# Optimization experiments

Measured on AMD Instinct MI355X. Metric: run time of the kernel, lower is better.

Reference implementation:

```python
import jax, jax.numpy as jnp
import numpy as np

B, K, D = 8, 1024, 512
H, DQ, DV = 8, 64, 64


def setup_inputs() -> dict:
    key = jax.random.key(0)
    ks = jax.random.split(key, 11)
    s = 0.02  # param init scale
    return {
        "query": jax.random.normal(ks[0], (B, K, D), jnp.float32),
        "key": jax.random.normal(ks[1], (B, K, D), jnp.float32),
        "value": jax.random.normal(ks[2], (B, K, D), jnp.float32),
        "Wq": jax.random.normal(ks[3], (D, H * DQ), jnp.float32) * s,
        "bq": jax.random.normal(ks[4], (H * DQ,), jnp.float32) * s,
        "Wk": jax.random.normal(ks[5], (D, H * DQ), jnp.float32) * s,
        "bk": jax.random.normal(ks[6], (H * DQ,), jnp.float32) * s,
        "Wv": jax.random.normal(ks[7], (D, H * DV), jnp.float32) * s,
        "bv": jax.random.normal(ks[8], (H * DV,), jnp.float32) * s,
        "Wo": jax.random.normal(ks[9], (H * DV, D), jnp.float32) * s,
        "bo": jax.random.normal(ks[10], (D,), jnp.float32) * s,
    }


def reference(query, key, value, Wq, bq, Wk, bk, Wv, bv, Wo, bo):
    b, k, _ = query.shape
    # Linear projections, split into heads: chunk(h, dim=-1) + cat(dim=0)
    # is equivalent to reshape (b, k, h, d) with head on a separate axis.
    q = (query @ Wq + bq).reshape(b, k, H, DQ)  # b k h dq
    kk = (key @ Wk + bk).reshape(b, k, H, DQ)   # b k h dq
    v = (value @ Wv + bv).reshape(b, k, H, DV)  # b k h dv
    # NOTE: original scales by sqrt(K) (sequence length), not sqrt(dq).
    scale = 1.0 / jnp.sqrt(jnp.asarray(k, q.dtype))
    scores = jnp.einsum("bqhd,bkhd->bhqk", q, kk) * scale
    attn = jax.nn.softmax(scores, axis=-1)
    ctx = jnp.einsum("bhqk,bkhd->bqhd", attn, v).reshape(b, k, H * DV)
    return ctx @ Wo + bo
```

## Files before the change

kernel.cpp:

```cpp
#include <hip/hip_runtime.h>
#include <hip/hip_bf16.h>

#define DEVI __device__ __forceinline__

typedef __attribute__((ext_vector_type(4))) float f32x4;
typedef __attribute__((ext_vector_type(8))) short bf16x8;

static constexpr int BB  = 8;
static constexpr int SEQ = 1024;
static constexpr int DIM = 512;
static constexpr int NH  = 8;
static constexpr int HD  = 64;
static constexpr int M   = BB * SEQ;


DEVI unsigned short f2bf(float x) {
  unsigned int u = __builtin_bit_cast(unsigned int, x);
  u += 0x7fffu + ((u >> 16) & 1u);
  return (unsigned short)(u >> 16);
}

DEVI float fexp2(float x) {
#if __has_builtin(__builtin_amdgcn_exp2f)
  return __builtin_amdgcn_exp2f(x);
#else
  float r; asm("v_exp_f32 %0, %1" : "=v"(r) : "v"(x)); return r;
#endif
}

DEVI void gload_lds16(const unsigned short* g, unsigned short* l) {
  __builtin_amdgcn_global_load_lds(
      (const __attribute__((address_space(1))) void*)g,
      (__attribute__((address_space(3))) void*)l, 16, 0, 0);
}

DEVI unsigned int cvtpk(float lo, float hi) {
  unsigned int r;
  asm("v_cvt_pk_bf16_f32 %0, %1, %2" : "=v"(r) : "v"(lo), "v"(hi));
  return r;
}


__global__ __launch_bounds__(256) void cvt_all_kernel(
    const float* __restrict__ q, const float* __restrict__ k, const float* __restrict__ v,
    unsigned short* __restrict__ oq, unsigned short* __restrict__ ok, unsigned short* __restrict__ ov,
    const float* __restrict__ w0, const float* __restrict__ w1,
    const float* __restrict__ w2, const float* __restrict__ w3,
    unsigned short* __restrict__ t0, unsigned short* __restrict__ t1,
    unsigned short* __restrict__ t2, unsigned short* __restrict__ t3) {
  __shared__ float tile[32][33];
  const int bid = blockIdx.x;
  if (bid < 12288) {
    const int z = bid >> 12;
    const int bl = bid & 4095;
    const float* in = (z == 0) ? q : ((z == 1) ? k : v);
    unsigned short* out = (z == 0) ? oq : ((z == 1) ? ok : ov);
    int i = (bl * 256 + threadIdx.x) * 4;
    float4 vv = *reinterpret_cast<const float4*>(in + i);
    ushort4 o;
    o.x = f2bf(vv.x); o.y = f2bf(vv.y); o.z = f2bf(vv.z); o.w = f2bf(vv.w);
    *reinterpret_cast<ushort4*>(out + i) = o;
  } else {
    const int id = bid - 12288;
    const int z = id >> 8;
    const int t = id & 255;
    const float* in = (z == 0) ? w0 : ((z == 1) ? w1 : ((z == 2) ? w2 : w3));
    unsigned short* out = (z == 0) ? t0 : ((z == 1) ? t1 : ((z == 2) ? t2 : t3));
    int n0 = (t & 15) * 32, k0 = (t >> 4) * 32;
    int tx = threadIdx.x & 31, ty = threadIdx.x >> 5;
#pragma unroll
    for (int r = 0; r < 32; r += 8)
      tile[ty + r][tx] = in[(size_t)(k0 + ty + r) * DIM + n0 + tx];
    __syncthreads();
#pragma unroll
    for (int r = 0; r < 32; r += 8)
      out[(size_t)(n0 + ty + r) * DIM + k0 + tx] = f2bf(tile[tx][ty + r]);
  }
}


__global__ __launch_bounds__(256) void gemm_proj(const unsigned short* __restrict__ Aq,
                                                 const unsigned short* __restrict__ Ak,
                                                 const unsigned short* __restrict__ Av,
                                                 const unsigned short* __restrict__ WqT,
                                                 const unsigned short* __restrict__ WkT,
                                                 const unsigned short* __restrict__ WvT,
                                                 const float* __restrict__ bq,
                                                 const float* __restrict__ bk,
                                                 const float* __restrict__ bv,
                                                 unsigned short* __restrict__ qb,
                                                 unsigned short* __restrict__ kb,
                                                 unsigned short* __restrict__ vT,
                                                 float qscale) {
  __shared__ unsigned short smem[24576];
  unsigned short* lA = smem;
  unsigned short* lB = smem + 12288;

  const int z = blockIdx.z;
  const unsigned short* A = (z == 0) ? Aq : ((z == 1) ? Ak : Av);
  const unsigned short* Bt = (z == 0) ? WqT : ((z == 1) ? WkT : WvT);
  const float* bias = (z == 0) ? bq : ((z == 1) ? bk : bv);
  const float gs = (z == 0) ? qscale : 1.0f;

  const int tid = threadIdx.x;
  const int lane = tid & 63, wave = tid >> 6;
  const int wr = wave >> 1, wc = wave & 1;
  const int row0 = blockIdx.x * 128, col0 = blockIdx.y * 128;
  const int lr = lane & 15, lg = lane >> 4;
  const int axor = (lr >> 1) & 3;
  const int cxr = lg ^ axor;

  f32x4 acc[4][4] = {};

  const int s0a = wave * 64;
  const int sA = s0a + lane, rA = sA >> 2;
  const int koA = ((sA & 3) ^ ((sA >> 3) & 3)) * 8;
  const int s0b = 256 + wave * 64;
  const int sB = s0b + lane, rB = sB >> 2;
  const int koB = ((sB & 3) ^ ((sB >> 3) & 3)) * 8;

#define GEMM_STAGE(buf, k0)                                                              \
  do {                                                                                   \
    gload_lds16(A + (size_t)(row0 + rA) * DIM + (k0) + koA, &lA[(buf)*4096 + s0a * 8]);  \
    gload_lds16(Bt + (size_t)(col0 + rA) * DIM + (k0) + koA, &lB[(buf)*4096 + s0a * 8]); \
    gload_lds16(A + (size_t)(row0 + rB) * DIM + (k0) + koB, &lA[(buf)*4096 + s0b * 8]);  \
    gload_lds16(Bt + (size_t)(col0 + rB) * DIM + (k0) + koB, &lB[(buf)*4096 + s0b * 8]); \
  } while (0)

#define GEMM_STEP(cur, VMC)                                                              \
  do {                                                                                   \
    asm volatile("s_waitcnt vmcnt(" #VMC ")" ::: "memory");                              \
    __builtin_amdgcn_s_barrier();                                                        \
    bf16x8 af[4], bfr[4];                                                                \
    _Pragma("unroll")                                                                    \
    for (int m = 0; m < 4; ++m)                                                          \
      af[m] = *reinterpret_cast<const bf16x8*>(&lA[(cur)*4096 + (wr * 64 + m * 16 + lr) * 32 + cxr * 8]); \
    _Pragma("unroll")                                                                    \
    for (int n = 0; n < 4; ++n)                                                          \
      bfr[n] = *reinterpret_cast<const bf16x8*>(&lB[(cur)*4096 + (wc * 64 + n * 16 + lr) * 32 + cxr * 8]); \
    __builtin_amdgcn_s_setprio(1);                                                       \
    _Pragma("unroll")                                                                    \
    for (int m = 0; m < 4; ++m)                                                          \
      _Pragma("unroll")                                                                  \
      for (int n = 0; n < 4; ++n)                                                        \
        acc[m][n] = __builtin_amdgcn_mfma_f32_16x16x32_bf16(af[m], bfr[n], acc[m][n], 0, 0, 0); \
    __builtin_amdgcn_s_setprio(0);                                                       \
    asm volatile("" ::: "memory");                                                       \
    __builtin_amdgcn_s_barrier();                                                        \
  } while (0)

  constexpr int NT = DIM / 32;
  GEMM_STAGE(0, 0);
  GEMM_STAGE(1, 32);
  for (int t = 0; t < NT - 2; ++t) {
    GEMM_STAGE((t + 2) % 3, (t + 2) * 32);
    GEMM_STEP(t % 3, 8);
  }
  GEMM_STEP((NT - 2) % 3, 4);
  GEMM_STEP((NT - 1) % 3, 0);
#undef GEMM_STAGE
#undef GEMM_STEP

  if (z < 2) {
    unsigned short* C = (z == 0) ? qb : kb;
#pragma unroll
    for (int m = 0; m < 4; ++m) {
#pragma unroll
      for (int n = 0; n < 4; ++n) {
        int col = col0 + wc * 64 + n * 16 + lr;
        int r0 = row0 + wr * 64 + m * 16 + lg * 4;
        float bvv = bias[col];
#pragma unroll
        for (int j = 0; j < 4; ++j)
          C[(size_t)(r0 + j) * DIM + col] = f2bf((acc[m][n][j] + bvv) * gs);
      }
    }
  } else {
    unsigned short* ldsT = smem;
    __syncthreads();
#pragma unroll
    for (int m = 0; m < 4; ++m) {
#pragma unroll
      for (int n = 0; n < 4; ++n) {
        const int col = wc * 64 + n * 16 + lr;
        const int r0l = wr * 64 + m * 16 + lg * 4;
        const float bvv = bias[col0 + col];
        ushort4 pk;
        pk.x = f2bf(acc[m][n][0] + bvv);
        pk.y = f2bf(acc[m][n][1] + bvv);
        pk.z = f2bf(acc[m][n][2] + bvv);
        pk.w = f2bf(acc[m][n][3] + bvv);
        *reinterpret_cast<ushort4*>(&ldsT[col * 136 + r0l]) = pk;
      }
    }
    __syncthreads();
    const int b = row0 >> 10, s_loc0 = row0 & 1023;
#pragma unroll
    for (int it = 0; it < 8; ++it) {
      int idx = it * 256 + tid;
      int c = idx >> 4, s8 = idx & 15;
      bf16x8 v = *reinterpret_cast<const bf16x8*>(&ldsT[c * 136 + s8 * 8]);
      *reinterpret_cast<bf16x8*>(
          vT + ((size_t)(b * DIM) + col0 + c) * SEQ + s_loc0 + s8 * 8) = v;
    }
  }
}


__global__ __launch_bounds__(256) void gemm_out(const unsigned short* __restrict__ A,
                                                const unsigned short* __restrict__ Bt,
                                                const float* __restrict__ bias,
                                                float* __restrict__ C) {
  __shared__ unsigned short lA[3][128 * 32];
  __shared__ unsigned short lB[3][128 * 32];
  const int tid = threadIdx.x;
  const int lane = tid & 63, wave = tid >> 6;
  const int wr = wave >> 1, wc = wave & 1;
  const int row0 = blockIdx.x * 128, col0 = blockIdx.y * 128;
  const int lr = lane & 15, lg = lane >> 4;
  const int axor = (lr >> 1) & 3;
  const int cxr = lg ^ axor;

  f32x4 acc[4][4] = {};

  const int s0a = wave * 64;
  const int sA = s0a + lane, rA = sA >> 2;
  const int koA = ((sA & 3) ^ ((sA >> 3) & 3)) * 8;
  const int s0b = 256 + wave * 64;
  const int sB = s0b + lane, rB = sB >> 2;
  const int koB = ((sB & 3) ^ ((sB >> 3) & 3)) * 8;

#define GEMM_STAGE(buf, k0)                                                        \
  do {                                                                             \
    gload_lds16(A + (size_t)(row0 + rA) * DIM + (k0) + koA, &lA[buf][s0a * 8]);    \
    gload_lds16(Bt + (size_t)(col0 + rA) * DIM + (k0) + koA, &lB[buf][s0a * 8]);   \
    gload_lds16(A + (size_t)(row0 + rB) * DIM + (k0) + koB, &lA[buf][s0b * 8]);    \
    gload_lds16(Bt + (size_t)(col0 + rB) * DIM + (k0) + koB, &lB[buf][s0b * 8]);   \
  } while (0)

#define GEMM_STEP(cur, VMC)                                                        \
  do {                                                                             \
    asm volatile("s_waitcnt vmcnt(" #VMC ")" ::: "memory");                        \
    __builtin_amdgcn_s_barrier();                                                  \
    bf16x8 af[4], bfr[4];                                                          \
    _Pragma("unroll")                                                              \
    for (int m = 0; m < 4; ++m)                                                    \
      af[m] = *reinterpret_cast<const bf16x8*>(&lA[cur][(wr * 64 + m * 16 + lr) * 32 + cxr * 8]); \
    _Pragma("unroll")                                                              \
    for (int n = 0; n < 4; ++n)                                                    \
      bfr[n] = *reinterpret_cast<const bf16x8*>(&lB[cur][(wc * 64 + n * 16 + lr) * 32 + cxr * 8]); \
    __builtin_amdgcn_s_setprio(1);                                                 \
    _Pragma("unroll")                                                              \
    for (int m = 0; m < 4; ++m)                                                    \
      _Pragma("unroll")                                                            \
      for (int n = 0; n < 4; ++n)                                                  \
        acc[m][n] = __builtin_amdgcn_mfma_f32_16x16x32_bf16(af[m], bfr[n], acc[m][n], 0, 0, 0); \
    __builtin_amdgcn_s_setprio(0);                                                 \
    asm volatile("" ::: "memory");                                                 \
    __builtin_amdgcn_s_barrier();                                                  \
  } while (0)

  constexpr int NT = DIM / 32;
  GEMM_STAGE(0, 0);
  GEMM_STAGE(1, 32);
  for (int t = 0; t < NT - 2; ++t) {
    GEMM_STAGE((t + 2) % 3, (t + 2) * 32);
    GEMM_STEP((t % 3), 8);
  }
  GEMM_STEP(((NT - 2) % 3), 4);
  GEMM_STEP(((NT - 1) % 3), 0);
#undef GEMM_STAGE
#undef GEMM_STEP

#pragma unroll
  for (int m = 0; m < 4; ++m) {
#pragma unroll
    for (int n = 0; n < 4; ++n) {
      int col = col0 + wc * 64 + n * 16 + lr;
      int r0 = row0 + wr * 64 + m * 16 + lg * 4;
      float bv = bias[col];
#pragma unroll
      for (int j = 0; j < 4; ++j)
        C[(size_t)(r0 + j) * DIM + col] = acc[m][n][j] + bv;
    }
  }
}


__global__ __launch_bounds__(512) void attn_kernel(const unsigned short* __restrict__ qb,
                                                   const unsigned short* __restrict__ kb,
                                                   const unsigned short* __restrict__ vT,
                                                   unsigned short* __restrict__ ctx) {
  __shared__ unsigned short lK[2][64 * 64];
  __shared__ unsigned short lV[2][64 * 64];
  __shared__ unsigned short Pl[8][16 * 72];

  const int b = blockIdx.x, h = blockIdx.y;
  const int tid = threadIdx.x, lane = tid & 63, wave = tid >> 6;
  const int lr = lane & 15, lg = lane >> 4;
  const int q0 = blockIdx.z * 128 + wave * 16;

  const int sr = tid >> 3, sc = (tid & 7) ^ (sr & 7);
  const int prK = ((sr & 15) << 2) | (sr >> 4);
  const unsigned short* Kbase = kb + ((size_t)b * SEQ) * DIM + (size_t)h * HD;
  const unsigned short* Vbase = vT + (size_t)(b * NH + h) * HD * SEQ;

  bf16x8 qf0, qf1;
  {
    const unsigned short* qrow = qb + ((size_t)(b * SEQ) + q0 + lr) * DIM + h * HD;
    qf0 = *reinterpret_cast<const bf16x8*>(qrow + lg * 8);
    qf1 = *reinterpret_cast<const bf16x8*>(qrow + 32 + lg * 8);
  }

  float l_r[4] = {0.f, 0.f, 0.f, 0.f};
  f32x4 o_acc[4];
#pragma unroll
  for (int n = 0; n < 4; ++n) o_acc[n] = f32x4{0.f, 0.f, 0.f, 0.f};

  unsigned short* pw = Pl[wave];

#define ATT_STAGE(buf, nk)                                                          \
  do {                                                                              \
    gload_lds16(Kbase + (size_t)((nk) + prK) * DIM + sc * 8, &lK[buf][(wave * 64) * 8]); \
    gload_lds16(Vbase + (size_t)sr * SEQ + (nk) + sc * 8, &lV[buf][(wave * 64) * 8]);   \
  } while (0)

#define ATT_COMPUTE(cur)                                                            \
  do {                                                                              \
    f32x4 st[4];                                                                    \
    __builtin_amdgcn_s_setprio(1);                                                  \
    _Pragma("unroll")                                                               \
    for (int kt = 0; kt < 4; ++kt) {                                                \
      const int row = kt * 16 + lr;                                                 \
      const char* rbase = (const char*)&lK[cur][0] + row * 128;                     \
      const int sw = (row & 7) << 4;                                                \
      bf16x8 kf0 = *reinterpret_cast<const bf16x8*>(rbase + ((lg * 16) ^ sw));      \
      bf16x8 kf1 = *reinterpret_cast<const bf16x8*>(rbase + ((64 + lg * 16) ^ sw)); \
      f32x4 a = {};                                                                 \
      a = __builtin_amdgcn_mfma_f32_16x16x32_bf16(qf0, kf0, a, 0, 0, 0);            \
      a = __builtin_amdgcn_mfma_f32_16x16x32_bf16(qf1, kf1, a, 0, 0, 0);            \
      st[kt] = a;                                                                   \
    }                                                                               \
    __builtin_amdgcn_s_setprio(0);                                                  \
    _Pragma("unroll")                                                               \
    for (int j = 0; j < 4; ++j) {                                                   \
      float p0 = fexp2(st[0][j]);                                                   \
      float p1 = fexp2(st[1][j]);                                                   \
      float p2 = fexp2(st[2][j]);                                                   \
      float p3 = fexp2(st[3][j]);                                                   \
      l_r[j] += (p0 + p1) + (p2 + p3);                                              \
      uint2 pkd;                                                                    \
      pkd.x = cvtpk(p0, p1);                                                        \
      pkd.y = cvtpk(p2, p3);                                                        \
      *reinterpret_cast<uint2*>((char*)pw + (lg * 4 + j) * 144 + lr * 8) = pkd;     \
    }                                                                               \
    _Pragma("unroll")                                                               \
    for (int c = 0; c < 2; ++c) {                                                   \
      bf16x8 pf = *reinterpret_cast<const bf16x8*>((const char*)pw + lr * 144 + c * 64 + lg * 16); \
      __builtin_amdgcn_s_setprio(1);                                                \
      _Pragma("unroll")                                                             \
      for (int n = 0; n < 4; ++n) {                                                 \
        const int row = n * 16 + lr;                                                \
        bf16x8 vf = *reinterpret_cast<const bf16x8*>(                               \
            (const char*)&lV[cur][0] + row * 128 + ((c * 64 + lg * 16) ^ ((row & 7) << 4))); \
        o_acc[n] = __builtin_amdgcn_mfma_f32_16x16x32_bf16(pf, vf, o_acc[n], 0, 0, 0); \
      }                                                                             \
      __builtin_amdgcn_s_setprio(0);                                                \
    }                                                                               \
  } while (0)

  constexpr int NTT = SEQ / 64;
  ATT_STAGE(0, 0);
  for (int t = 0; t < NTT - 1; ++t) {
    const int cur = t & 1;
    ATT_STAGE(cur ^ 1, (t + 1) * 64);
    asm volatile("s_waitcnt vmcnt(2)" ::: "memory");
    __builtin_amdgcn_s_barrier();
    ATT_COMPUTE(cur);
    asm volatile("" ::: "memory");
    __builtin_amdgcn_s_barrier();
  }
  asm volatile("s_waitcnt vmcnt(0)" ::: "memory");
  __builtin_amdgcn_s_barrier();
  ATT_COMPUTE((NTT - 1) & 1);
#undef ATT_STAGE
#undef ATT_COMPUTE

  float invl[4];
#pragma unroll
  for (int j = 0; j < 4; ++j) {
    float l = l_r[j];
#pragma unroll
    for (int msk = 1; msk < 16; msk <<= 1) l += __shfl_xor(l, msk);
    invl[j] = 1.f / l;
  }
#pragma unroll
  for (int n = 0; n < 4; ++n)
#pragma unroll
    for (int j = 0; j < 4; ++j)
      pw[(lg * 4 + j) * 72 + n * 16 + lr] = f2bf(o_acc[n][j] * invl[j]);

#pragma unroll
  for (int it = 0; it < 2; ++it) {
    int idx = it * 64 + lane;
    int r = idx >> 3, cc = idx & 7;
    bf16x8 v = *reinterpret_cast<const bf16x8*>((const char*)pw + r * 144 + cc * 16);
    *reinterpret_cast<bf16x8*>(ctx + ((size_t)(b * SEQ) + q0 + r) * DIM + h * HD + cc * 8) = v;
  }
}


extern "C" void kernel_launch(void* const* d_in, const int* in_sizes, int n_in,
                              void* d_out, int out_size, void* d_ws, size_t ws_size,
                              hipStream_t stream) {
  const float* query = (const float*)d_in[0];
  const float* key_  = (const float*)d_in[1];
  const float* value = (const float*)d_in[2];
  const float* Wq = (const float*)d_in[3];
  const float* bq = (const float*)d_in[4];
  const float* Wk = (const float*)d_in[5];
  const float* bk = (const float*)d_in[6];
  const float* Wv = (const float*)d_in[7];
  const float* bv = (const float*)d_in[8];
  const float* Wo = (const float*)d_in[9];
  const float* bo = (const float*)d_in[10];
  float* out = (float*)d_out;

  unsigned short* ws = (unsigned short*)d_ws;
  const size_t NM = (size_t)M * DIM;
  const size_t NW = (size_t)DIM * DIM;
  unsigned short* xq   = ws;
  unsigned short* xk   = xq + NM;
  unsigned short* xv   = xk + NM;
  unsigned short* qb   = xv + NM;
  unsigned short* kbuf = qb + NM;
  unsigned short* vTb  = kbuf + NM;
  unsigned short* ctx  = vTb + NM;
  unsigned short* Wqt  = ctx + NM;
  unsigned short* Wkt  = Wqt + NW;
  unsigned short* Wvt  = Wkt + NW;
  unsigned short* Wot  = Wvt + NW;

  cvt_all_kernel<<<13312, 256, 0, stream>>>(query, key_, value, xq, xk, xv,
                                            Wq, Wk, Wv, Wo, Wqt, Wkt, Wvt, Wot);

  const float qscale = 0.03125f * 1.4426950408889634f;
  gemm_proj<<<dim3(M / 128, DIM / 128, 3), 256, 0, stream>>>(
      xq, xk, xv, Wqt, Wkt, Wvt, bq, bk, bv, qb, kbuf, vTb, qscale);

  attn_kernel<<<dim3(BB, NH, SEQ / 128), 512, 0, stream>>>(qb, kbuf, vTb, ctx);

  gemm_out<<<dim3(M / 128, DIM / 128), 256, 0, stream>>>(ctx, Wot, bo, out);
}
```

Baseline: 72.03 us.

## Deepen GEMM pipelines to four LDS stages with one barrier per step

Both projection and output GEMMs move from a 3-buffer LDS ring to a 4-buffer ring, prefetching three k-tiles ahead. Each iteration now issues its next stage after a single wait+barrier instead of two barriers around the MFMA block, because the fourth buffer removes the write-after-read hazard. This cuts barrier overhead and gives loads more time in flight. In exchange, LDS use per block rises (64KB for the A/B tiles), which may reduce how many blocks fit on a CU.

```diff
diff --git a/kernel.cpp b/kernel.cpp
--- a/kernel.cpp
+++ b/kernel.cpp
@@ -92,9 +92,9 @@
                                                  unsigned short* __restrict__ kb,
                                                  unsigned short* __restrict__ vT,
                                                  float qscale) {
-  __shared__ unsigned short smem[24576];
+  __shared__ unsigned short smem[32768];
   unsigned short* lA = smem;
-  unsigned short* lB = smem + 12288;
+  unsigned short* lB = smem + 16384;
 
   const int z = blockIdx.z;
   const unsigned short* A = (z == 0) ? Aq : ((z == 1) ? Ak : Av);
@@ -127,10 +127,8 @@
     gload_lds16(Bt + (size_t)(col0 + rB) * DIM + (k0) + koB, &lB[(buf)*4096 + s0b * 8]); \
   } while (0)
 
-#define GEMM_STEP(cur, VMC)                                                              \
+#define GEMM_MFMA(cur)                                                                   \
   do {                                                                                   \
-    asm volatile("s_waitcnt vmcnt(" #VMC ")" ::: "memory");                              \
-    __builtin_amdgcn_s_barrier();                                                        \
     bf16x8 af[4], bfr[4];                                                                \
     _Pragma("unroll")                                                                    \
     for (int m = 0; m < 4; ++m)                                                          \
@@ -145,21 +143,33 @@
       for (int n = 0; n < 4; ++n)                                                        \
         acc[m][n] = __builtin_amdgcn_mfma_f32_16x16x32_bf16(af[m], bfr[n], acc[m][n], 0, 0, 0); \
     __builtin_amdgcn_s_setprio(0);                                                       \
+  } while (0)
+
+#define GEMM_SYNC(VMC)                                                                   \
+  do {                                                                                   \
+    asm volatile("s_waitcnt vmcnt(" #VMC ")" ::: "memory");                              \
+    __builtin_amdgcn_s_barrier();                                                        \
     asm volatile("" ::: "memory");                                                       \
-    __builtin_amdgcn_s_barrier();                                                        \
   } while (0)
 
   constexpr int NT = DIM / 32;
   GEMM_STAGE(0, 0);
   GEMM_STAGE(1, 32);
-  for (int t = 0; t < NT - 2; ++t) {
-    GEMM_STAGE((t + 2) % 3, (t + 2) * 32);
-    GEMM_STEP(t % 3, 8);
-  }
-  GEMM_STEP((NT - 2) % 3, 4);
-  GEMM_STEP((NT - 1) % 3, 0);
+  GEMM_STAGE(2, 64);
+  for (int t = 0; t < NT - 3; ++t) {
+    GEMM_SYNC(8);
+    GEMM_STAGE((t + 3) & 3, (t + 3) * 32);
+    GEMM_MFMA(t & 3);
+  }
+  GEMM_SYNC(8);
+  GEMM_MFMA((NT - 3) & 3);
+  GEMM_SYNC(4);
+  GEMM_MFMA((NT - 2) & 3);
+  GEMM_SYNC(0);
+  GEMM_MFMA((NT - 1) & 3);
 #undef GEMM_STAGE
-#undef GEMM_STEP
+#undef GEMM_MFMA
+#undef GEMM_SYNC
 
   if (z < 2) {
     unsigned short* C = (z == 0) ? qb : kb;
@@ -211,8 +221,8 @@
                                                 const unsigned short* __restrict__ Bt,
                                                 const float* __restrict__ bias,
                                                 float* __restrict__ C) {
-  __shared__ unsigned short lA[3][128 * 32];
-  __shared__ unsigned short lB[3][128 * 32];
+  __shared__ unsigned short lA[4][128 * 32];
+  __shared__ unsigned short lB[4][128 * 32];
   const int tid = threadIdx.x;
   const int lane = tid & 63, wave = tid >> 6;
   const int wr = wave >> 1, wc = wave & 1;
@@ -238,10 +248,8 @@
     gload_lds16(Bt + (size_t)(col0 + rB) * DIM + (k0) + koB, &lB[buf][s0b * 8]);   \
   } while (0)
 
-#define GEMM_STEP(cur, VMC)                                                        \
+#define GEMM_MFMA(cur)                                                             \
   do {                                                                             \
-    asm volatile("s_waitcnt vmcnt(" #VMC ")" ::: "memory");                        \
-    __builtin_amdgcn_s_barrier();                                                  \
     bf16x8 af[4], bfr[4];                                                          \
     _Pragma("unroll")                                                              \
     for (int m = 0; m < 4; ++m)                                                    \
@@ -256,21 +264,33 @@
       for (int n = 0; n < 4; ++n)                                                  \
         acc[m][n] = __builtin_amdgcn_mfma_f32_16x16x32_bf16(af[m], bfr[n], acc[m][n], 0, 0, 0); \
     __builtin_amdgcn_s_setprio(0);                                                 \
+  } while (0)
+
+#define GEMM_SYNC(VMC)                                                             \
+  do {                                                                             \
+    asm volatile("s_waitcnt vmcnt(" #VMC ")" ::: "memory");                        \
+    __builtin_amdgcn_s_barrier();                                                  \
     asm volatile("" ::: "memory");                                                 \
-    __builtin_amdgcn_s_barrier();                                                  \
   } while (0)
 
   constexpr int NT = DIM / 32;
   GEMM_STAGE(0, 0);
   GEMM_STAGE(1, 32);
-  for (int t = 0; t < NT - 2; ++t) {
-    GEMM_STAGE((t + 2) % 3, (t + 2) * 32);
-    GEMM_STEP((t % 3), 8);
-  }
-  GEMM_STEP(((NT - 2) % 3), 4);
-  GEMM_STEP(((NT - 1) % 3), 0);
+  GEMM_STAGE(2, 64);
+  for (int t = 0; t < NT - 3; ++t) {
+    GEMM_SYNC(8);
+    GEMM_STAGE((t + 3) & 3, (t + 3) * 32);
+    GEMM_MFMA(t & 3);
+  }
+  GEMM_SYNC(8);
+  GEMM_MFMA((NT - 3) & 3);
+  GEMM_SYNC(4);
+  GEMM_MFMA((NT - 2) & 3);
+  GEMM_SYNC(0);
+  GEMM_MFMA((NT - 1) & 3);
 #undef GEMM_STAGE
-#undef GEMM_STEP
+#undef GEMM_MFMA
+#undef GEMM_SYNC
 
 #pragma unroll
   for (int m = 0; m < 4; ++m) {
```

Result: no change. 71.63 us (median of 2 runs) (-0.5%).
